# Optimization experiments

Measured on AMD Instinct MI355X. Metric: run time of the kernel, lower is better.

The kernel has to match this reference:

```python
import jax, jax.numpy as jnp
import numpy as np

N_NODES = 100000
N_EDGES = 640000
D_IN = 128
D_OUT = 128


def setup_inputs() -> dict:
    key = jax.random.key(0)
    k1, k2, k3, k4 = jax.random.split(key, 4)
    x = jax.random.normal(k1, (N_NODES, D_IN), dtype=jnp.float32)
    edge_index = jax.random.randint(k2, (2, N_EDGES), 0, N_NODES, dtype=jnp.int64)
    W = jax.random.normal(k3, (D_OUT, D_IN), dtype=jnp.float32) * 0.05
    b = jax.random.normal(k4, (D_OUT,), dtype=jnp.float32) * 0.05
    return {"x": x, "edge_index": edge_index, "W": W, "b": b}


def reference(x, edge_index, W, b):
    src, dst = edge_index[0], edge_index[1]
    n = x.shape[0]
    ones = jnp.ones(src.shape[0], dtype=x.dtype)
    # degree counts both endpoints of every edge (matches the two scatter_adds)
    deg = jax.ops.segment_sum(ones, src, num_segments=n) + \
          jax.ops.segment_sum(ones, dst, num_segments=n)
    deg_inv_sqrt = jnp.where(deg > 0, jax.lax.rsqrt(deg), 0.0)
    norm = deg_inv_sqrt[src] * deg_inv_sqrt[dst]  # [E]
    # symmetric message passing: out[d] += norm*x[s]; out[s] += norm*x[d]
    msg_to_dst = norm[:, None] * x[src]  # [E, D]
    msg_to_src = norm[:, None] * x[dst]  # [E, D]
    out = x + jax.ops.segment_sum(msg_to_dst, dst, num_segments=n) + \
              jax.ops.segment_sum(msg_to_src, src, num_segments=n)
    return jax.nn.relu(out @ W.T + b)
```

## Files before the change

kernel.cpp:

```cpp
#include <hip/hip_runtime.h>

#define D 128
#define EPB 4096


__global__ __launch_bounds__(256) void k_bin1(const int* __restrict__ ei,
                                              int* __restrict__ bh,
                                              int E, int NB) {
    __shared__ int h[512];
    int t = threadIdx.x;
    for (int i = t; i < 512; i += 256) h[i] = 0;
    __syncthreads();
    int e0 = blockIdx.x * EPB;
#pragma unroll
    for (int i = 0; i < EPB / 256; ++i) {
        int e = e0 + i * 256 + t;
        if (e < E) {
            atomicAdd(&h[ei[e] >> 8], 1);
            atomicAdd(&h[ei[E + e] >> 8], 1);
        }
    }
    __syncthreads();
    for (int i = t; i < NB; i += 256) bh[(size_t)blockIdx.x * NB + i] = h[i];
}

__global__ __launch_bounds__(256) void k_bin2(int* __restrict__ bh,
                                              int* __restrict__ btot,
                                              int nblk, int NB) {
    __shared__ int s[256];
    __shared__ int carry;
    int k = blockIdx.x, t = threadIdx.x;
    if (t == 0) carry = 0;
    __syncthreads();
    for (int c0 = 0; c0 < nblk; c0 += 256) {
        int b = c0 + t;
        int v = (b < nblk) ? bh[(size_t)b * NB + k] : 0;
        s[t] = v;
        __syncthreads();
#pragma unroll
        for (int off = 1; off < 256; off <<= 1) {
            int a = (t >= off) ? s[t - off] : 0;
            __syncthreads();
            s[t] += a;
            __syncthreads();
        }
        int incl = s[t];
        int mybase = carry;
        __syncthreads();
        if (b < nblk) bh[(size_t)b * NB + k] = mybase + incl - v;
        if (t == 255) carry = mybase + incl;
        __syncthreads();
    }
    if (t == 0) btot[k] = carry;
}

__global__ __launch_bounds__(512) void k_bin2b(const int* __restrict__ btot,
                                               int* __restrict__ bbase, int NB) {
    __shared__ int s[512];
    int t = threadIdx.x;
    int v = (t < NB) ? btot[t] : 0;
    s[t] = v;
    __syncthreads();
#pragma unroll
    for (int off = 1; off < 512; off <<= 1) {
        int a = (t >= off) ? s[t - off] : 0;
        __syncthreads();
        s[t] += a;
        __syncthreads();
    }
    if (t < NB) {
        bbase[t] = s[t] - v;
        if (t == NB - 1) bbase[NB] = s[t];
    }
}

__global__ __launch_bounds__(256) void k_bin3(const int* __restrict__ ei,
                                              const int* __restrict__ bh,
                                              const int* __restrict__ bbase,
                                              unsigned int* __restrict__ rec,
                                              int E, int NB) {
    __shared__ int cur[512];
    int t = threadIdx.x;
    for (int i = t; i < NB; i += 256)
        cur[i] = bbase[i] + bh[(size_t)blockIdx.x * NB + i];
    __syncthreads();
    int e0 = blockIdx.x * EPB;
#pragma unroll
    for (int i = 0; i < EPB / 256; ++i) {
        int e = e0 + i * 256 + t;
        if (e < E) {
            unsigned int u = (unsigned int)ei[e];
            unsigned int d = (unsigned int)ei[E + e];
            int p = atomicAdd(&cur[u >> 8], 1);
            rec[p] = ((u & 255u) << 24) | d;
            int q = atomicAdd(&cur[d >> 8], 1);
            rec[q] = ((d & 255u) << 24) | u;
        }
    }
}

__global__ __launch_bounds__(256) void k_bucket(const unsigned int* __restrict__ rec,
                                                const int* __restrict__ bbase,
                                                int* __restrict__ offsets,
                                                float* __restrict__ dis,
                                                int* __restrict__ nbr,
                                                int n, int NB) {
    __shared__ int dcnt[256];
    __shared__ int sc[256];
    int k = blockIdx.x, t = threadIdx.x;
    int rbeg = bbase[k], rend = bbase[k + 1];
    dcnt[t] = 0;
    __syncthreads();
    for (int i = rbeg + t; i < rend; i += 256)
        atomicAdd(&dcnt[rec[i] >> 24], 1);
    __syncthreads();
    int v = dcnt[t];
    sc[t] = v;
    __syncthreads();
#pragma unroll
    for (int off = 1; off < 256; off <<= 1) {
        int a = (t >= off) ? sc[t - off] : 0;
        __syncthreads();
        sc[t] += a;
        __syncthreads();
    }
    int excl = rbeg + sc[t] - v;
    int node = (k << 8) + t;
    if (node < n) {
        offsets[node] = excl;
        dis[node] = v > 0 ? rsqrtf((float)v) : 0.f;
    }
    if (k == NB - 1 && t == 0) offsets[n] = rend;
    sc[t] = excl;
    __syncthreads();
    for (int i = rbeg + t; i < rend; i += 256) {
        unsigned int r = rec[i];
        int p = atomicAdd(&sc[r >> 24], 1);
        nbr[p] = (int)(r & 0xFFFFFFu);
    }
}

__global__ __launch_bounds__(256) void k_cvtwt(const float* __restrict__ x,
                                               unsigned int* __restrict__ xb, int n2,
                                               const float* __restrict__ W,
                                               float* __restrict__ Wt, int cvtb) {
    if ((int)blockIdx.x >= cvtb) {
        __shared__ float tile[32][33];
        int bid = blockIdx.x - cvtb;
        int bx = bid & 3, by = bid >> 2;
        int c = threadIdx.x & 31, r = threadIdx.x >> 5;
#pragma unroll
        for (int i = 0; i < 4; ++i)
            tile[r + 8 * i][c] = W[(size_t)(by * 32 + r + 8 * i) * D + bx * 32 + c];
        __syncthreads();
#pragma unroll
        for (int i = 0; i < 4; ++i)
            Wt[(size_t)(bx * 32 + r + 8 * i) * D + by * 32 + c] = tile[c][r + 8 * i];
        return;
    }
    int i = blockIdx.x * 256 + threadIdx.x;
    if (i < n2) {
        float2 v = *(const float2*)(x + (size_t)i * 2);
        unsigned int u0 = __float_as_uint(v.x);
        unsigned int u1 = __float_as_uint(v.y);
        u0 += 0x7fffu + ((u0 >> 16) & 1u);
        u1 += 0x7fffu + ((u1 >> 16) & 1u);
        xb[i] = (u0 >> 16) | (u1 & 0xffff0000u);
    }
}

__device__ __forceinline__ float bflo(unsigned int a) { return __uint_as_float(a << 16); }
__device__ __forceinline__ float bfhi(unsigned int a) { return __uint_as_float(a & 0xffff0000u); }

__global__ __launch_bounds__(256) void k_gather2(const int* __restrict__ offsets,
                                                 const int* __restrict__ nbr,
                                                 const float* __restrict__ x,
                                                 const unsigned int* __restrict__ xb,
                                                 const float* __restrict__ dis,
                                                 float* __restrict__ out, int n) {
    int wid = blockIdx.x * 4 + (threadIdx.x >> 6);
    int nodeA = wid * 2;
    if (nodeA >= n) return;
    int nodeB = nodeA + 1;
    bool hasB = nodeB < n;
    int lane = threadIdx.x & 63;

    int begA = offsets[nodeA], endA = offsets[nodeA + 1];
    int begB = hasB ? offsets[nodeB] : 0;
    int endB = hasB ? offsets[nodeB + 1] : 0;
    float dvA = dis[nodeA];
    float dvB = hasB ? dis[nodeB] : 0.f;

    float axA = 0.f, ayA = 0.f, axB = 0.f, ayB = 0.f;
    int baseA = begA, baseB = begB;
    while (baseA < endA || baseB < endB) {
        int cntA = endA - baseA; cntA = cntA < 0 ? 0 : (cntA > 64 ? 64 : cntA);
        int cntB = endB - baseB; cntB = cntB < 0 ? 0 : (cntB > 64 ? 64 : cntB);
        int uidA = (lane < cntA) ? nbr[baseA + lane] : 0;
        int uidB = (lane < cntB) ? nbr[baseB + lane] : 0;
        float duA = (lane < cntA) ? dis[uidA] : 0.f;
        float duB = (lane < cntB) ? dis[uidB] : 0.f;
        int m = cntA > cntB ? cntA : cntB;

        for (int k = 0; k < m; k += 4) {
            int uA0 = __shfl(uidA, k + 0, 64); float nA0 = dvA * __shfl(duA, k + 0, 64);
            int uA1 = __shfl(uidA, k + 1, 64); float nA1 = dvA * __shfl(duA, k + 1, 64);
            int uA2 = __shfl(uidA, k + 2, 64); float nA2 = dvA * __shfl(duA, k + 2, 64);
            int uA3 = __shfl(uidA, k + 3, 64); float nA3 = dvA * __shfl(duA, k + 3, 64);
            int uB0 = __shfl(uidB, k + 0, 64); float nB0 = dvB * __shfl(duB, k + 0, 64);
            int uB1 = __shfl(uidB, k + 1, 64); float nB1 = dvB * __shfl(duB, k + 1, 64);
            int uB2 = __shfl(uidB, k + 2, 64); float nB2 = dvB * __shfl(duB, k + 2, 64);
            int uB3 = __shfl(uidB, k + 3, 64); float nB3 = dvB * __shfl(duB, k + 3, 64);
            unsigned int aA0 = xb[(size_t)uA0 * 64 + lane];
            unsigned int aA1 = xb[(size_t)uA1 * 64 + lane];
            unsigned int aA2 = xb[(size_t)uA2 * 64 + lane];
            unsigned int aA3 = xb[(size_t)uA3 * 64 + lane];
            unsigned int aB0 = xb[(size_t)uB0 * 64 + lane];
            unsigned int aB1 = xb[(size_t)uB1 * 64 + lane];
            unsigned int aB2 = xb[(size_t)uB2 * 64 + lane];
            unsigned int aB3 = xb[(size_t)uB3 * 64 + lane];
            axA = fmaf(nA0, bflo(aA0), axA); ayA = fmaf(nA0, bfhi(aA0), ayA);
            axA = fmaf(nA1, bflo(aA1), axA); ayA = fmaf(nA1, bfhi(aA1), ayA);
            axA = fmaf(nA2, bflo(aA2), axA); ayA = fmaf(nA2, bfhi(aA2), ayA);
            axA = fmaf(nA3, bflo(aA3), axA); ayA = fmaf(nA3, bfhi(aA3), ayA);
            axB = fmaf(nB0, bflo(aB0), axB); ayB = fmaf(nB0, bfhi(aB0), ayB);
            axB = fmaf(nB1, bflo(aB1), axB); ayB = fmaf(nB1, bfhi(aB1), ayB);
            axB = fmaf(nB2, bflo(aB2), axB); ayB = fmaf(nB2, bfhi(aB2), ayB);
            axB = fmaf(nB3, bflo(aB3), axB); ayB = fmaf(nB3, bfhi(aB3), ayB);
        }
        baseA += 64;
        baseB += 64;
    }

    const float2 xvA = *(const float2*)(x + (size_t)nodeA * D + lane * 2);
    *(float2*)(out + (size_t)nodeA * D + lane * 2) =
        make_float2(axA + xvA.x, ayA + xvA.y);
    if (hasB) {
        const float2 xvB = *(const float2*)(x + (size_t)nodeB * D + lane * 2);
        *(float2*)(out + (size_t)nodeB * D + lane * 2) =
            make_float2(axB + xvB.x, ayB + xvB.y);
    }
}

__global__ __launch_bounds__(256) void k_gemm(const float* __restrict__ Wt_g,
                                              const float* __restrict__ b,
                                              float* __restrict__ out, int n) {
    __shared__ float Wh[64][D];
    __shared__ float h[64][132];
    int tid = threadIdx.x;
    int oc = (tid & 31) * 4;
    int rr = (tid >> 5) * 8;
    int row0 = blockIdx.x * 64;

#pragma unroll
    for (int i = 0; i < 8; ++i) {
        int idx = tid + 256 * i;
        int r = idx >> 5;
        int c = (idx & 31) * 4;
        int rg = row0 + r;
        float4 hv = make_float4(0.f, 0.f, 0.f, 0.f);
        if (rg < n) hv = *(const float4*)(out + (size_t)rg * D + c);
        *(float4*)&h[r][c] = hv;
    }

    float4 b4 = *(const float4*)(b + oc);
    float acc[8][4];
#pragma unroll
    for (int j = 0; j < 8; ++j) {
        acc[j][0] = b4.x; acc[j][1] = b4.y; acc[j][2] = b4.z; acc[j][3] = b4.w;
    }

#pragma unroll
    for (int p = 0; p < 2; ++p) {
        __syncthreads();
#pragma unroll
        for (int i = 0; i < 8; ++i) {
            int idx = tid + 256 * i;
            int kr = idx >> 5;
            int o4 = (idx & 31) * 4;
            *(float4*)&Wh[kr][o4] = *(const float4*)(Wt_g + (size_t)(p * 64 + kr) * D + o4);
        }
        __syncthreads();

        for (int k = 0; k < 64; k += 4) {
            float4 w0 = *(const float4*)&Wh[k + 0][oc];
            float4 w1 = *(const float4*)&Wh[k + 1][oc];
            float4 w2 = *(const float4*)&Wh[k + 2][oc];
            float4 w3 = *(const float4*)&Wh[k + 3][oc];
#pragma unroll
            for (int j = 0; j < 8; ++j) {
                float4 h4 = *(const float4*)&h[rr + j][p * 64 + k];
                acc[j][0] = fmaf(h4.x, w0.x, acc[j][0]);
                acc[j][1] = fmaf(h4.x, w0.y, acc[j][1]);
                acc[j][2] = fmaf(h4.x, w0.z, acc[j][2]);
                acc[j][3] = fmaf(h4.x, w0.w, acc[j][3]);
                acc[j][0] = fmaf(h4.y, w1.x, acc[j][0]);
                acc[j][1] = fmaf(h4.y, w1.y, acc[j][1]);
                acc[j][2] = fmaf(h4.y, w1.z, acc[j][2]);
                acc[j][3] = fmaf(h4.y, w1.w, acc[j][3]);
                acc[j][0] = fmaf(h4.z, w2.x, acc[j][0]);
                acc[j][1] = fmaf(h4.z, w2.y, acc[j][1]);
                acc[j][2] = fmaf(h4.z, w2.z, acc[j][2]);
                acc[j][3] = fmaf(h4.z, w2.w, acc[j][3]);
                acc[j][0] = fmaf(h4.w, w3.x, acc[j][0]);
                acc[j][1] = fmaf(h4.w, w3.y, acc[j][1]);
                acc[j][2] = fmaf(h4.w, w3.z, acc[j][2]);
                acc[j][3] = fmaf(h4.w, w3.w, acc[j][3]);
            }
        }
    }

#pragma unroll
    for (int j = 0; j < 8; ++j) {
        int rg = row0 + rr + j;
        if (rg < n) {
            float4 r4 = make_float4(fmaxf(acc[j][0], 0.f), fmaxf(acc[j][1], 0.f),
                                    fmaxf(acc[j][2], 0.f), fmaxf(acc[j][3], 0.f));
            *(float4*)(out + (size_t)rg * D + oc) = r4;
        }
    }
}

extern "C" void kernel_launch(void* const* d_in, const int* in_sizes, int n_in,
                              void* d_out, int out_size, void* d_ws, size_t ws_size,
                              hipStream_t stream) {
    const float* x  = (const float*)d_in[0];
    const int*   ei = (const int*)d_in[1];
    const float* W  = (const float*)d_in[2];
    const float* b  = (const float*)d_in[3];
    float* out = (float*)d_out;

    int E = in_sizes[1] / 2;
    int n = in_sizes[0] / D;
    int NB = (n + 255) >> 8;
    int nblk = (E + EPB - 1) / EPB;

    int* ws = (int*)d_ws;
    int* bh    = ws;
    int* btot  = ws + (size_t)nblk * NB;
    int* bbase = btot + NB;
    unsigned int* rec = (unsigned int*)(bbase + NB + 1);
    unsigned int* xb = (unsigned int*)ws;
    int*   offsets = ws + (size_t)n * 64;
    float* dis     = (float*)(offsets + n + 1);
    int*   nbr     = (int*)(dis + n);
    float* Wt_g    = (float*)(nbr + (size_t)2 * E);

    k_bin1<<<nblk, 256, 0, stream>>>(ei, bh, E, NB);
    k_bin2<<<NB, 256, 0, stream>>>(bh, btot, nblk, NB);
    k_bin2b<<<1, 512, 0, stream>>>(btot, bbase, NB);
    k_bin3<<<nblk, 256, 0, stream>>>(ei, bh, bbase, rec, E, NB);
    k_bucket<<<NB, 256, 0, stream>>>(rec, bbase, offsets, dis, nbr, n, NB);
    int n2 = n * 64;
    int cvtb = (n2 + 255) / 256;
    k_cvtwt<<<cvtb + 16, 256, 0, stream>>>(x, xb, n2, W, Wt_g, cvtb);
    k_gather2<<<((n + 1) / 2 + 3) / 4, 256, 0, stream>>>(offsets, nbr, x, xb, dis, out, n);
    k_gemm<<<(n + 63) / 64, 256, 0, stream>>>(Wt_g, b, out, n);
}
```

Baseline: 254.1 us.

## Fuse gather with bf16 MFMA GEMM and merge preprocessing kernels

Replaces the separate gather and FP32 SIMT GEMM with one fused kernel. Each 512-thread block aggregates 16 rows into LDS as bf16, then runs a 16x16x32 bf16 MFMA against a bf16 copy of W, which removes the FP32 round-trip of the intermediate through global memory. The histogram, x conversion and W conversion are merged into one launch. Buckets shrink to 128 nodes, and the bucket kernel stages records in LDS and sorts in place, dropping the separate nbr array. The trade-offs are lower precision, since both the aggregated features and W are now bf16, and a hard 8192-record LDS cap per bucket that silently truncates larger buckets.

```diff
diff --git a/kernel.cpp b/kernel.cpp
--- a/kernel.cpp
+++ b/kernel.cpp
@@ -3,29 +3,57 @@
 #define D 128
 #define EPB 4096
 
-
-__global__ __launch_bounds__(256) void k_bin1(const int* __restrict__ ei,
-                                              int* __restrict__ bh,
-                                              int E, int NB) {
-    __shared__ int h[512];
-    int t = threadIdx.x;
-    for (int i = t; i < 512; i += 256) h[i] = 0;
-    __syncthreads();
-    int e0 = blockIdx.x * EPB;
-#pragma unroll
-    for (int i = 0; i < EPB / 256; ++i) {
-        int e = e0 + i * 256 + t;
-        if (e < E) {
-            atomicAdd(&h[ei[e] >> 8], 1);
-            atomicAdd(&h[ei[E + e] >> 8], 1);
-        }
-    }
-    __syncthreads();
-    for (int i = t; i < NB; i += 256) bh[(size_t)blockIdx.x * NB + i] = h[i];
-}
-
-__global__ __launch_bounds__(256) void k_bin2(int* __restrict__ bh,
-                                              int* __restrict__ btot,
+typedef __attribute__((ext_vector_type(8))) short short8;
+typedef __attribute__((ext_vector_type(4))) float f32x4;
+
+__device__ __forceinline__ unsigned int pack_bf16(float a, float b) {
+    unsigned int u0 = __float_as_uint(a);
+    unsigned int u1 = __float_as_uint(b);
+    u0 += 0x7fffu + ((u0 >> 16) & 1u);
+    u1 += 0x7fffu + ((u1 >> 16) & 1u);
+    return (u0 >> 16) | (u1 & 0xffff0000u);
+}
+__device__ __forceinline__ float bflo(unsigned int a) { return __uint_as_float(a << 16); }
+__device__ __forceinline__ float bfhi(unsigned int a) { return __uint_as_float(a & 0xffff0000u); }
+
+__global__ __launch_bounds__(256) void k_pre(const int* __restrict__ ei, int* __restrict__ bh,
+                                             int E, int NB, int nblk,
+                                             const float* __restrict__ x,
+                                             unsigned int* __restrict__ xb, int n2, int cvtb,
+                                             const float* __restrict__ W,
+                                             unsigned int* __restrict__ Wb) {
+    int bid = blockIdx.x, t = threadIdx.x;
+    if (bid < nblk) {
+        __shared__ int h[1024];
+        for (int i = t; i < NB; i += 256) h[i] = 0;
+        __syncthreads();
+        int e0 = bid * EPB;
+#pragma unroll
+        for (int i = 0; i < EPB / 256; ++i) {
+            int e = e0 + i * 256 + t;
+            if (e < E) {
+                atomicAdd(&h[ei[e] >> 7], 1);
+                atomicAdd(&h[ei[E + e] >> 7], 1);
+            }
+        }
+        __syncthreads();
+        for (int i = t; i < NB; i += 256) bh[(size_t)bid * NB + i] = h[i];
+    } else if (bid < nblk + cvtb) {
+        int i = (bid - nblk) * 256 + t;
+        if (i < n2) {
+            float2 v = *(const float2*)(x + (size_t)i * 2);
+            xb[i] = pack_bf16(v.x, v.y);
+        }
+    } else {
+        int j = (bid - nblk - cvtb) * 256 + t;
+        if (j < D * D / 2) {
+            float2 v = *(const float2*)(W + (size_t)j * 2);
+            Wb[j] = pack_bf16(v.x, v.y);
+        }
+    }
+}
+
+__global__ __launch_bounds__(256) void k_bin2(int* __restrict__ bh, int* __restrict__ btot,
                                               int nblk, int NB) {
     __shared__ int s[256];
     __shared__ int carry;
@@ -54,15 +82,15 @@
     if (t == 0) btot[k] = carry;
 }
 
-__global__ __launch_bounds__(512) void k_bin2b(const int* __restrict__ btot,
-                                               int* __restrict__ bbase, int NB) {
-    __shared__ int s[512];
+__global__ __launch_bounds__(1024) void k_bin2b(const int* __restrict__ btot,
+                                                int* __restrict__ bbase, int NB) {
+    __shared__ int s[1024];
     int t = threadIdx.x;
     int v = (t < NB) ? btot[t] : 0;
     s[t] = v;
     __syncthreads();
 #pragma unroll
-    for (int off = 1; off < 512; off <<= 1) {
+    for (int off = 1; off < 1024; off <<= 1) {
         int a = (t >= off) ? s[t - off] : 0;
         __syncthreads();
         s[t] += a;
@@ -79,7 +107,7 @@
                                               const int* __restrict__ bbase,
                                               unsigned int* __restrict__ rec,
                                               int E, int NB) {
-    __shared__ int cur[512];
+    __shared__ int cur[1024];
     int t = threadIdx.x;
     for (int i = t; i < NB; i += 256)
         cur[i] = bbase[i] + bh[(size_t)blockIdx.x * NB + i];
@@ -91,105 +119,76 @@
         if (e < E) {
             unsigned int u = (unsigned int)ei[e];
             unsigned int d = (unsigned int)ei[E + e];
-            int p = atomicAdd(&cur[u >> 8], 1);
-            rec[p] = ((u & 255u) << 24) | d;
-            int q = atomicAdd(&cur[d >> 8], 1);
-            rec[q] = ((d & 255u) << 24) | u;
-        }
-    }
-}
-
-__global__ __launch_bounds__(256) void k_bucket(const unsigned int* __restrict__ rec,
+            int p = atomicAdd(&cur[u >> 7], 1);
+            rec[p] = ((u & 127u) << 25) | d;
+            int q = atomicAdd(&cur[d >> 7], 1);
+            rec[q] = ((d & 127u) << 25) | u;
+        }
+    }
+}
+
+__global__ __launch_bounds__(256) void k_bucket(unsigned int* __restrict__ rec,
                                                 const int* __restrict__ bbase,
                                                 int* __restrict__ offsets,
                                                 float* __restrict__ dis,
-                                                int* __restrict__ nbr,
                                                 int n, int NB) {
-    __shared__ int dcnt[256];
-    __shared__ int sc[256];
+    __shared__ unsigned int lrec[8192];
+    __shared__ int dcnt[128], sc[128];
     int k = blockIdx.x, t = threadIdx.x;
     int rbeg = bbase[k], rend = bbase[k + 1];
-    dcnt[t] = 0;
-    __syncthreads();
-    for (int i = rbeg + t; i < rend; i += 256)
-        atomicAdd(&dcnt[rec[i] >> 24], 1);
-    __syncthreads();
-    int v = dcnt[t];
-    sc[t] = v;
-    __syncthreads();
-#pragma unroll
-    for (int off = 1; off < 256; off <<= 1) {
-        int a = (t >= off) ? sc[t - off] : 0;
-        __syncthreads();
-        sc[t] += a;
-        __syncthreads();
-    }
-    int excl = rbeg + sc[t] - v;
-    int node = (k << 8) + t;
-    if (node < n) {
-        offsets[node] = excl;
-        dis[node] = v > 0 ? rsqrtf((float)v) : 0.f;
-    }
-    if (k == NB - 1 && t == 0) offsets[n] = rend;
-    sc[t] = excl;
-    __syncthreads();
-    for (int i = rbeg + t; i < rend; i += 256) {
-        unsigned int r = rec[i];
-        int p = atomicAdd(&sc[r >> 24], 1);
-        nbr[p] = (int)(r & 0xFFFFFFu);
-    }
-}
-
-__global__ __launch_bounds__(256) void k_cvtwt(const float* __restrict__ x,
-                                               unsigned int* __restrict__ xb, int n2,
-                                               const float* __restrict__ W,
-                                               float* __restrict__ Wt, int cvtb) {
-    if ((int)blockIdx.x >= cvtb) {
-        __shared__ float tile[32][33];
-        int bid = blockIdx.x - cvtb;
-        int bx = bid & 3, by = bid >> 2;
-        int c = threadIdx.x & 31, r = threadIdx.x >> 5;
-#pragma unroll
-        for (int i = 0; i < 4; ++i)
-            tile[r + 8 * i][c] = W[(size_t)(by * 32 + r + 8 * i) * D + bx * 32 + c];
-        __syncthreads();
-#pragma unroll
-        for (int i = 0; i < 4; ++i)
-            Wt[(size_t)(bx * 32 + r + 8 * i) * D + by * 32 + c] = tile[c][r + 8 * i];
-        return;
-    }
-    int i = blockIdx.x * 256 + threadIdx.x;
-    if (i < n2) {
-        float2 v = *(const float2*)(x + (size_t)i * 2);
-        unsigned int u0 = __float_as_uint(v.x);
-        unsigned int u1 = __float_as_uint(v.y);
-        u0 += 0x7fffu + ((u0 >> 16) & 1u);
-        u1 += 0x7fffu + ((u1 >> 16) & 1u);
-        xb[i] = (u0 >> 16) | (u1 & 0xffff0000u);
-    }
-}
-
-__device__ __forceinline__ float bflo(unsigned int a) { return __uint_as_float(a << 16); }
-__device__ __forceinline__ float bfhi(unsigned int a) { return __uint_as_float(a & 0xffff0000u); }
-
-__global__ __launch_bounds__(256) void k_gather2(const int* __restrict__ offsets,
-                                                 const int* __restrict__ nbr,
-                                                 const float* __restrict__ x,
-                                                 const unsigned int* __restrict__ xb,
-                                                 const float* __restrict__ dis,
-                                                 float* __restrict__ out, int n) {
-    int wid = blockIdx.x * 4 + (threadIdx.x >> 6);
-    int nodeA = wid * 2;
-    if (nodeA >= n) return;
-    int nodeB = nodeA + 1;
-    bool hasB = nodeB < n;
-    int lane = threadIdx.x & 63;
-
-    int begA = offsets[nodeA], endA = offsets[nodeA + 1];
-    int begB = hasB ? offsets[nodeB] : 0;
-    int endB = hasB ? offsets[nodeB + 1] : 0;
-    float dvA = dis[nodeA];
-    float dvB = hasB ? dis[nodeB] : 0.f;
+    int nrec = rend - rbeg;
+    if (nrec > 8192) nrec = 8192;
+    for (int i = t; i < nrec; i += 256) lrec[i] = rec[rbeg + i];
+    if (t < 128) dcnt[t] = 0;
+    __syncthreads();
+    for (int i = t; i < nrec; i += 256) atomicAdd(&dcnt[lrec[i] >> 25], 1);
+    __syncthreads();
+    int v = (t < 128) ? dcnt[t] : 0;
+    if (t < 128) sc[t] = v;
+    __syncthreads();
+#pragma unroll
+    for (int off = 1; off < 128; off <<= 1) {
+        int a = (t >= off && t < 128) ? sc[t - off] : 0;
+        __syncthreads();
+        if (t < 128) sc[t] += a;
+        __syncthreads();
+    }
+    if (t < 128) {
+        int excl = rbeg + sc[t] - v;
+        int node = (k << 7) + t;
+        if (node < n) {
+            offsets[node] = excl;
+            dis[node] = v > 0 ? rsqrtf((float)v) : 0.f;
+            if (node == n - 1) offsets[n] = rend;
+        }
+        sc[t] = excl;
+    }
+    __syncthreads();
+    for (int i = t; i < nrec; i += 256) {
+        unsigned int r = lrec[i];
+        int p = atomicAdd(&sc[r >> 25], 1);
+        rec[p] = r & 0x1FFFFFFu;
+    }
+}
+
+__global__ __launch_bounds__(512) void k_fused(const int* __restrict__ offsets,
+                                               const int* __restrict__ nbr,
+                                               const unsigned int* __restrict__ xb,
+                                               const float* __restrict__ dis,
+                                               const unsigned int* __restrict__ Wb,
+                                               const float* __restrict__ bias,
+                                               float* __restrict__ out, int n) {
+    __shared__ unsigned int hl[16 * 64];
+    int tid = threadIdx.x;
+    int wave = tid >> 6, lane = tid & 63;
+    int row0 = blockIdx.x * 16;
+    int nodeA = row0 + wave * 2, nodeB = nodeA + 1;
+    bool hasA = nodeA < n, hasB = nodeB < n;
+
+    int begA = 0, endA = 0, begB = 0, endB = 0;
+    float dvA = 0.f, dvB = 0.f;
+    if (hasA) { begA = offsets[nodeA]; endA = offsets[nodeA + 1]; dvA = dis[nodeA]; }
+    if (hasB) { begB = offsets[nodeB]; endB = offsets[nodeB + 1]; dvB = dis[nodeB]; }
 
     float axA = 0.f, ayA = 0.f, axB = 0.f, ayB = 0.f;
     int baseA = begA, baseB = begB;
@@ -201,7 +200,6 @@
         float duA = (lane < cntA) ? dis[uidA] : 0.f;
         float duB = (lane < cntB) ? dis[uidB] : 0.f;
         int m = cntA > cntB ? cntA : cntB;
-
         for (int k = 0; k < m; k += 4) {
             int uA0 = __shfl(uidA, k + 0, 64); float nA0 = dvA * __shfl(duA, k + 0, 64);
             int uA1 = __shfl(uidA, k + 1, 64); float nA1 = dvA * __shfl(duA, k + 1, 64);
@@ -232,92 +230,31 @@
         baseB += 64;
     }
 
-    const float2 xvA = *(const float2*)(x + (size_t)nodeA * D + lane * 2);
-    *(float2*)(out + (size_t)nodeA * D + lane * 2) =
-        make_float2(axA + xvA.x, ayA + xvA.y);
-    if (hasB) {
-        const float2 xvB = *(const float2*)(x + (size_t)nodeB * D + lane * 2);
-        *(float2*)(out + (size_t)nodeB * D + lane * 2) =
-            make_float2(axB + xvB.x, ayB + xvB.y);
-    }
-}
-
-__global__ __launch_bounds__(256) void k_gemm(const float* __restrict__ Wt_g,
-                                              const float* __restrict__ b,
-                                              float* __restrict__ out, int n) {
-    __shared__ float Wh[64][D];
-    __shared__ float h[64][132];
-    int tid = threadIdx.x;
-    int oc = (tid & 31) * 4;
-    int rr = (tid >> 5) * 8;
-    int row0 = blockIdx.x * 64;
-
-#pragma unroll
-    for (int i = 0; i < 8; ++i) {
-        int idx = tid + 256 * i;
-        int r = idx >> 5;
-        int c = (idx & 31) * 4;
-        int rg = row0 + r;
-        float4 hv = make_float4(0.f, 0.f, 0.f, 0.f);
-        if (rg < n) hv = *(const float4*)(out + (size_t)rg * D + c);
-        *(float4*)&h[r][c] = hv;
-    }
-
-    float4 b4 = *(const float4*)(b + oc);
-    float acc[8][4];
-#pragma unroll
-    for (int j = 0; j < 8; ++j) {
-        acc[j][0] = b4.x; acc[j][1] = b4.y; acc[j][2] = b4.z; acc[j][3] = b4.w;
-    }
-
-#pragma unroll
-    for (int p = 0; p < 2; ++p) {
-        __syncthreads();
-#pragma unroll
-        for (int i = 0; i < 8; ++i) {
-            int idx = tid + 256 * i;
-            int kr = idx >> 5;
-            int o4 = (idx & 31) * 4;
-            *(float4*)&Wh[kr][o4] = *(const float4*)(Wt_g + (size_t)(p * 64 + kr) * D + o4);
-        }
-        __syncthreads();
-
-        for (int k = 0; k < 64; k += 4) {
-            float4 w0 = *(const float4*)&Wh[k + 0][oc];
-            float4 w1 = *(const float4*)&Wh[k + 1][oc];
-            float4 w2 = *(const float4*)&Wh[k + 2][oc];
-            float4 w3 = *(const float4*)&Wh[k + 3][oc];
-#pragma unroll
-            for (int j = 0; j < 8; ++j) {
-                float4 h4 = *(const float4*)&h[rr + j][p * 64 + k];
-                acc[j][0] = fmaf(h4.x, w0.x, acc[j][0]);
-                acc[j][1] = fmaf(h4.x, w0.y, acc[j][1]);
-                acc[j][2] = fmaf(h4.x, w0.z, acc[j][2]);
-                acc[j][3] = fmaf(h4.x, w0.w, acc[j][3]);
-                acc[j][0] = fmaf(h4.y, w1.x, acc[j][0]);
-                acc[j][1] = fmaf(h4.y, w1.y, acc[j][1]);
-                acc[j][2] = fmaf(h4.y, w1.z, acc[j][2]);
-                acc[j][3] = fmaf(h4.y, w1.w, acc[j][3]);
-                acc[j][0] = fmaf(h4.z, w2.x, acc[j][0]);
-                acc[j][1] = fmaf(h4.z, w2.y, acc[j][1]);
-                acc[j][2] = fmaf(h4.z, w2.z, acc[j][2]);
-                acc[j][3] = fmaf(h4.z, w2.w, acc[j][3]);
-                acc[j][0] = fmaf(h4.w, w3.x, acc[j][0]);
-                acc[j][1] = fmaf(h4.w, w3.y, acc[j][1]);
-                acc[j][2] = fmaf(h4.w, w3.z, acc[j][2]);
-                acc[j][3] = fmaf(h4.w, w3.w, acc[j][3]);
-            }
-        }
-    }
-
-#pragma unroll
-    for (int j = 0; j < 8; ++j) {
-        int rg = row0 + rr + j;
-        if (rg < n) {
-            float4 r4 = make_float4(fmaxf(acc[j][0], 0.f), fmaxf(acc[j][1], 0.f),
-                                    fmaxf(acc[j][2], 0.f), fmaxf(acc[j][3], 0.f));
-            *(float4*)(out + (size_t)rg * D + oc) = r4;
-        }
+    unsigned int hA = 0u, hB = 0u;
+    if (hasA) { unsigned int xr = xb[(size_t)nodeA * 64 + lane]; hA = pack_bf16(axA + bflo(xr), ayA + bfhi(xr)); }
+    if (hasB) { unsigned int xr = xb[(size_t)nodeB * 64 + lane]; hB = pack_bf16(axB + bflo(xr), ayB + bfhi(xr)); }
+    int rA = wave * 2, rB = rA + 1;
+    hl[rA * 64 + (lane ^ ((rA & 7) << 2))] = hA;
+    hl[rB * 64 + (lane ^ ((rB & 7) << 2))] = hB;
+    __syncthreads();
+
+    int l15 = lane & 15, l4 = lane >> 4;
+    f32x4 acc = {0.f, 0.f, 0.f, 0.f};
+    const uint4* wb4 = (const uint4*)Wb;
+#pragma unroll
+    for (int ks = 0; ks < 4; ++ks) {
+        int aw = l15 * 64 + ((ks * 16 + l4 * 4) ^ ((l15 & 7) << 2));
+        uint4 av = *(const uint4*)&hl[aw];
+        uint4 bv = wb4[(wave * 16 + l15) * 16 + ks * 4 + l4];
+        union { uint4 u; short8 s; } ua, ub;
+        ua.u = av; ub.u = bv;
+        acc = __builtin_amdgcn_mfma_f32_16x16x32_bf16(ua.s, ub.s, acc, 0, 0, 0);
+    }
+    float bs = bias[wave * 16 + l15];
+#pragma unroll
+    for (int r = 0; r < 4; ++r) {
+        int rg = row0 + l4 * 4 + r;
+        if (rg < n) out[(size_t)rg * D + wave * 16 + l15] = fmaxf(acc[r] + bs, 0.f);
     }
 }
 
@@ -332,28 +269,28 @@
 
     int E = in_sizes[1] / 2;
     int n = in_sizes[0] / D;
-    int NB = (n + 255) >> 8;
+    int NB = (n + 127) >> 7;
     int nblk = (E + EPB - 1) / EPB;
 
-    int* ws = (int*)d_ws;
-    int* bh    = ws;
-    int* btot  = ws + (size_t)nblk * NB;
-    int* bbase = btot + NB;
-    unsigned int* rec = (unsigned int*)(bbase + NB + 1);
-    unsigned int* xb = (unsigned int*)ws;
-    int*   offsets = ws + (size_t)n * 64;
-    float* dis     = (float*)(offsets + n + 1);
-    int*   nbr     = (int*)(dis + n);
-    float* Wt_g    = (float*)(nbr + (size_t)2 * E);
-
-    k_bin1<<<nblk, 256, 0, stream>>>(ei, bh, E, NB);
-    k_bin2<<<NB, 256, 0, stream>>>(bh, btot, nblk, NB);
-    k_bin2b<<<1, 512, 0, stream>>>(btot, bbase, NB);
-    k_bin3<<<nblk, 256, 0, stream>>>(ei, bh, bbase, rec, E, NB);
-    k_bucket<<<NB, 256, 0, stream>>>(rec, bbase, offsets, dis, nbr, n, NB);
+    unsigned int* ws = (unsigned int*)d_ws;
+    size_t off = 0;
+    unsigned int* xb  = ws + off;  off += (size_t)n * 64;
+    unsigned int* rec = ws + off;  off += (size_t)2 * E;
+    int* bh    = (int*)(ws + off); off += (size_t)nblk * NB;
+    int* btot  = (int*)(ws + off); off += NB;
+    int* bbase = (int*)(ws + off); off += NB + 1;
+    int* offsets = (int*)(ws + off); off += n + 1;
+    float* dis = (float*)(ws + off); off += n;
+    unsigned int* Wb = ws + off;   off += D * D / 2;
+
     int n2 = n * 64;
     int cvtb = (n2 + 255) / 256;
-    k_cvtwt<<<cvtb + 16, 256, 0, stream>>>(x, xb, n2, W, Wt_g, cvtb);
-    k_gather2<<<((n + 1) / 2 + 3) / 4, 256, 0, stream>>>(offsets, nbr, x, xb, dis, out, n);
-    k_gemm<<<(n + 63) / 64, 256, 0, stream>>>(Wt_g, b, out, n);
-}
+    int wbb = (D * D / 2 + 255) / 256;
+
+    k_pre<<<nblk + cvtb + wbb, 256, 0, stream>>>(ei, bh, E, NB, nblk, x, xb, n2, cvtb, W, Wb);
+    k_bin2<<<NB, 256, 0, stream>>>(bh, btot, nblk, NB);
+    k_bin2b<<<1, 1024, 0, stream>>>(btot, bbase, NB);
+    k_bin3<<<nblk, 256, 0, stream>>>(ei, bh, bbase, rec, E, NB);
+    k_bucket<<<NB, 256, 0, stream>>>(rec, bbase, offsets, dis, n, NB);
+    k_fused<<<(n + 15) / 16, 512, 0, stream>>>(offsets, (const int*)rec, xb, dis, Wb, b, out, n);
+}
```

New measurement: 211.4 us. -16.8%, faster.
